# Kernel optimization log

Measured on AMD Instinct MI355X. Metric: run time of the kernel, lower is better.

## Reference

```python
import jax, jax.numpy as jnp
import numpy as np

N_EXPERTS, D_MODEL, D_FF = 8, 1024, 2048
N_TOKENS, TOP_K = 4 * 2048, 2


def setup_inputs() -> dict:
    key = jax.random.key(0)
    ks = jax.random.split(key, 6)
    std = (1.0 / 3.0) ** 0.5
    return {
        "x": jax.random.normal(ks[0], (4, 2048, D_MODEL), dtype=jnp.float32),
        "expert_indices": jax.random.randint(ks[1], (N_TOKENS, TOP_K), 0, N_EXPERTS, dtype=jnp.int64),
        "expert_weights": jax.random.uniform(ks[2], (N_TOKENS, TOP_K), dtype=jnp.float32),
        "w1": jax.random.normal(ks[3], (N_EXPERTS, D_MODEL, D_FF), dtype=jnp.float32) * (std / D_MODEL ** 0.5),
        "w2": jax.random.normal(ks[4], (N_EXPERTS, D_MODEL, D_FF), dtype=jnp.float32) * (std / D_MODEL ** 0.5),
        "w3": jax.random.normal(ks[5], (N_EXPERTS, D_FF, D_MODEL), dtype=jnp.float32) * (std / D_FF ** 0.5),
    }


def reference(x, expert_indices, expert_weights, w1, w2, w3):
    input_shape = x.shape
    d = x.shape[-1]
    xt = x.reshape(-1, d)                      # [N, d_model]
    n_tokens = xt.shape[0]
    n_experts = w1.shape[0]
    # Dense routing matrix [N, E]: sum of top-k weights per (token, expert).
    # Equivalent to the original's per-pair scatter (index_add) combine.
    route = jnp.zeros((n_tokens, n_experts), dtype=xt.dtype)
    route = route.at[jnp.arange(n_tokens)[:, None], expert_indices].add(expert_weights)

    def step(acc, ws):
        w1e, w2e, w3e, re = ws
        hidden = jax.nn.silu(xt @ w1e) * (xt @ w2e)   # SwiGLU [N, d_ff]
        return acc + re[:, None] * (hidden @ w3e), None

    out, _ = jax.lax.scan(step, jnp.zeros_like(xt), (w1, w2, w3, route.T))
    return out.reshape(input_shape)
```

## Files before the change

### kernel.cpp

```cpp
#include <hip/hip_runtime.h>
#include <cstdint>

typedef unsigned short u16;
typedef u16 u16x8 __attribute__((ext_vector_type(8)));
typedef __bf16 bf16x8 __attribute__((ext_vector_type(8)));
typedef float f32x4 __attribute__((ext_vector_type(4)));

#define DEV static __device__ __forceinline__

constexpr int NT = 8192;
constexpr int NP = NT * 2;
constexpr int NE = 8;
constexpr int DM = 1024;
constexpr int DF = 2048;
constexpr int MAXS = 17664;
constexpr int MAXT256 = 71;
constexpr int MAXT128 = 136;
constexpr int NWG1 = 8 * 142;
constexpr int NWG2 = 8 * MAXT128;
constexpr int NTRANS = 24 * 512;
constexpr int NPREP = MAXS + NTRANS;

DEV u16 f2bf(float f) {
  uint32_t u = __builtin_bit_cast(uint32_t, f);
  u += 0x7fffu + ((u >> 16) & 1u);
  return (u16)(u >> 16);
}

DEV void gload16(const void* g, void* l) {
  __builtin_amdgcn_global_load_lds((const __attribute__((address_space(1))) void*)g,
                                   (__attribute__((address_space(3))) void*)l, 16, 0, 0);
}

DEV bf16x8 ldfrag(const char* p) { return __builtin_bit_cast(bf16x8, *(const u16x8*)p); }

DEV f32x4 MFMA(bf16x8 a, bf16x8 b, f32x4 c) {
  return __builtin_amdgcn_mfma_f32_16x16x32_bf16(a, b, c, 0, 0, 0);
}

__global__ void k_route(const int* __restrict__ eidx, const float* __restrict__ ew,
                        int* meta, int* slot_token, float* slot_weight, int* pair_slot) {
  __shared__ int cnt[NE], cur[NE], off[NE];
  const int tid = threadIdx.x;
  if (tid < NE) { cnt[tid] = 0; cur[tid] = 0; }
  __syncthreads();
  for (int p = tid; p < NP; p += 1024) atomicAdd(&cnt[eidx[p] & 7], 1);
  __syncthreads();
  if (tid == 0) {
    int o = 0, t2 = 0, t1 = 0;
    for (int e = 0; e < NE; ++e) {
      off[e] = o; meta[e] = cnt[e]; meta[16 + e] = o;
      const int c = cnt[e];
      o += ((c + 127) >> 7) << 7;
      for (int mt = 0; mt * 256 < c; ++mt) meta[32 + t2++] = e | (mt << 8);
      for (int mt = 0; mt * 128 < c; ++mt) meta[128 + t1++] = e | (mt << 8);
    }
    meta[24] = o; meta[25] = t2; meta[26] = t1;
  }
  __syncthreads();
  for (int s = tid; s < MAXS; s += 1024) slot_token[s] = -1;
  __syncthreads();
  for (int p = tid; p < NP; p += 1024) {
    const int e = eidx[p] & 7;
    const int pos = off[e] + atomicAdd(&cur[e], 1);
    slot_token[pos]  = p >> 1;
    slot_weight[pos] = ew[p];
    pair_slot[p] = pos;
  }
}

__global__ void k_prep(const float* __restrict__ x, const int* __restrict__ slot_token,
                       u16* __restrict__ Xg,
                       const float* __restrict__ w1, const float* __restrict__ w2,
                       const float* __restrict__ w3, u16* __restrict__ w1T,
                       u16* __restrict__ w2T, u16* __restrict__ w3T) {
  __shared__ u16 tile[64][72];
  const int bid = blockIdx.x;
  const int t = threadIdx.x;

  if (bid < MAXS) {
    const int tok = slot_token[bid];
    const int c = t * 4;
    alignas(8) u16 b[4] = {0, 0, 0, 0};
    if (tok >= 0) {
      const float4 v = *reinterpret_cast<const float4*>(x + (size_t)tok * DM + c);
      b[0] = f2bf(v.x); b[1] = f2bf(v.y); b[2] = f2bf(v.z); b[3] = f2bf(v.w);
    }
    *reinterpret_cast<uint2*>(Xg + (size_t)bid * DM + c) = *reinterpret_cast<const uint2*>(b);
    return;
  }

  const int fid = bid - MAXS;
  const int z = fid >> 9;
  const int id = fid & 511;
  const int which = z >> 3, e = z & 7;
  const float* s; u16* d; int K, N, n0, k0;
  const size_t mo = (size_t)e * DM * DF;
  if (which == 0)      { s = w1 + mo; d = w1T + mo; K = DM; N = DF; n0 = (id & 31) * 64; k0 = (id >> 5) * 64; }
  else if (which == 1) { s = w2 + mo; d = w2T + mo; K = DM; N = DF; n0 = (id & 31) * 64; k0 = (id >> 5) * 64; }
  else                 { s = w3 + mo; d = w3T + mo; K = DF; N = DM; n0 = (id & 15) * 64; k0 = (id >> 4) * 64; }

  const int r = t >> 4, cb = (t & 15) * 4;
#pragma unroll
  for (int it = 0; it < 4; ++it) {
    const float4 v = *reinterpret_cast<const float4*>(s + (size_t)(k0 + r + it * 16) * N + n0 + cb);
    tile[r + it * 16][cb + 0] = f2bf(v.x);
    tile[r + it * 16][cb + 1] = f2bf(v.y);
    tile[r + it * 16][cb + 2] = f2bf(v.z);
    tile[r + it * 16][cb + 3] = f2bf(v.w);
  }
  __syncthreads();
  const int nl = t >> 2, ks = (t & 3) * 16;
  alignas(16) u16 vals[16];
#pragma unroll
  for (int j = 0; j < 16; ++j) vals[j] = tile[ks + j][nl];
  u16* dp = d + (size_t)(n0 + nl) * K + k0 + ks;
  *reinterpret_cast<uint4*>(dp)     = *reinterpret_cast<const uint4*>(vals);
  *reinterpret_cast<uint4*>(dp + 8) = *reinterpret_cast<const uint4*>(vals + 8);
}

__global__ __launch_bounds__(512, 2)
void k_gemm1(const u16* __restrict__ Xg, const u16* __restrict__ w1T, const u16* __restrict__ w2T,
             u16* __restrict__ H, const int* __restrict__ meta) {
  const int bid = blockIdx.x;
  const int xcd = bid & 7;
  const int local = bid >> 3;
  const int ti = local >> 1;
  if (ti >= meta[25]) return;
  const int n0 = (xcd * 2 + (local & 1)) * 128;
  const int ent = meta[32 + ti];
  const int e = ent & 255, mt = ent >> 8;
  const int base = meta[16 + e];
  const int cntp = meta[17 + e] - base;

  __shared__ __align__(16) char sm[2][65536];

  const int tid = threadIdx.x;
  const int lane = tid & 63;
  const int w = tid >> 6;
  const int wr = w >> 2, wc = w & 3;
  const int lrow = lane & 15, lk = lane >> 4;
  const int SX = lrow & 7;
  int cofs[2];
  cofs[0] = ((0 * 4 + lk) ^ SX) * 16;
  cofs[1] = ((1 * 4 + lk) ^ SX) * 16;
  const int Abase  = (wr * 128 + lrow) * 128;
  const int B1base = 32768 + (wc * 32 + lrow) * 128;
  const int B2base = B1base + 16384;

  const int srow8 = tid >> 3;
  const int scolw = ((tid & 7) ^ (srow8 & 7)) * 16;

  const char* AgT = (const char*)(Xg + (size_t)(base + mt * 256) * DM) + (size_t)srow8 * 2048 + scolw;
  const char* B1T = (const char*)(w1T + ((size_t)e * DF + n0) * DM)    + (size_t)srow8 * 2048 + scolw;
  const char* B2T = (const char*)(w2T + ((size_t)e * DF + n0) * DM)    + (size_t)srow8 * 2048 + scolw;

  f32x4 acc1[8][2] = {};
  f32x4 acc2[8][2] = {};

  auto SP = [&](char* d, size_t kb, int q) {
    switch (q) {
      case 0: gload16(AgT + kb,          d + tid * 16);
              gload16(AgT + 131072 + kb, d + 8192  + tid * 16); break;
      case 1: gload16(AgT + 262144 + kb, d + 16384 + tid * 16);
              gload16(AgT + 393216 + kb, d + 24576 + tid * 16); break;
      case 2: gload16(B1T + kb,          d + 32768 + tid * 16);
              gload16(B1T + 131072 + kb, d + 40960 + tid * 16); break;
      case 3: gload16(B2T + kb,          d + 49152 + tid * 16);
              gload16(B2T + 131072 + kb, d + 57344 + tid * 16); break;
    }
  };

  bf16x8 b1f[2][2], b2f[2][2];

  auto LDA4 = [&](const char* s, int mh, int ks, bf16x8* a) {
#pragma unroll
    for (int j = 0; j < 4; ++j)
      a[j] = ldfrag(s + Abase + mh * 8192 + j * 2048 + cofs[ks]);
  };
  auto MF16 = [&](int mh, int ks, const bf16x8* a) {
    __builtin_amdgcn_s_setprio(1);
#pragma unroll
    for (int j = 0; j < 4; ++j)
#pragma unroll
      for (int n = 0; n < 2; ++n) {
        acc1[mh * 4 + j][n] = MFMA(a[j], b1f[n][ks], acc1[mh * 4 + j][n]);
        acc2[mh * 4 + j][n] = MFMA(a[j], b2f[n][ks], acc2[mh * 4 + j][n]);
      }
    __builtin_amdgcn_s_setprio(0);
  };

  SP(sm[0], 0, 0); SP(sm[0], 0, 1); SP(sm[0], 0, 2); SP(sm[0], 0, 3);

  for (int kt = 0; kt < 16; ++kt) {
    const char* s = sm[kt & 1];
    char* d = sm[(kt + 1) & 1];
    const size_t kbn = (size_t)((kt + 1 < 16) ? kt + 1 : 15) * 128;
    bf16x8 a[4];

    SP(d, kbn, 0);
    asm volatile("s_waitcnt vmcnt(2)" ::: "memory");
    __builtin_amdgcn_s_barrier();
#pragma unroll
    for (int n = 0; n < 2; ++n)
#pragma unroll
      for (int s2 = 0; s2 < 2; ++s2) {
        b1f[n][s2] = ldfrag(s + B1base + n * 2048 + cofs[s2]);
        b2f[n][s2] = ldfrag(s + B2base + n * 2048 + cofs[s2]);
      }
    LDA4(s, 0, 0, a);
    MF16(0, 0, a);
    __builtin_amdgcn_s_barrier();

    LDA4(s, 1, 0, a);
    SP(d, kbn, 1);
    __builtin_amdgcn_s_barrier();
    MF16(1, 0, a);
    __builtin_amdgcn_s_barrier();

    LDA4(s, 0, 1, a);
    SP(d, kbn, 2);
    __builtin_amdgcn_s_barrier();
    MF16(0, 1, a);
    __builtin_amdgcn_s_barrier();

    LDA4(s, 1, 1, a);
    SP(d, kbn, 3);
    __builtin_amdgcn_s_barrier();
    MF16(1, 1, a);
    __builtin_amdgcn_s_barrier();
  }

  u16* Hrow = H + (size_t)(base + mt * 256) * DF + n0;
#pragma unroll
  for (int m = 0; m < 8; ++m)
#pragma unroll
    for (int r = 0; r < 4; ++r) {
      const int rloc = wr * 128 + m * 16 + lk * 4 + r;
      if (mt * 256 + rloc >= cntp) continue;
      u16* hp = Hrow + (size_t)rloc * DF + wc * 32 + lrow;
#pragma unroll
      for (int n = 0; n < 2; ++n) {
        const float h1 = acc1[m][n][r], h2 = acc2[m][n][r];
        const float sv = h1 / (1.f + __expf(-h1)) * h2;
        hp[n * 16] = f2bf(sv);
      }
    }
}

__global__ __launch_bounds__(256, 2)
void k_gemm2(const u16* __restrict__ H, const u16* __restrict__ w3T, const int* __restrict__ meta,
             const float* __restrict__ slot_weight, u16* __restrict__ O) {
  const int bid = blockIdx.x;
  const int ti = bid >> 3;
  if (ti >= meta[26]) return;
  const int n0 = (bid & 7) * 128;
  const int ent = meta[128 + ti];
  const int e = ent & 255, mt = ent >> 8;
  const int base = meta[16 + e];

  __shared__ __align__(16) char sm[2][32768];

  const int tid = threadIdx.x;
  const int lane = tid & 63;
  const int w = tid >> 6;
  const int wr = w >> 1, wc = w & 1;
  const int lrow = lane & 15, lk = lane >> 4;
  const int SX = lrow & 7;
  int cofs[2];
  cofs[0] = ((0 * 4 + lk) ^ SX) * 16;
  cofs[1] = ((1 * 4 + lk) ^ SX) * 16;
  const int Abase = (wr * 64 + lrow) * 128;
  const int Bbase = 16384 + (wc * 64 + lrow) * 128;

  const int srow = tid >> 3;
  const int scolw = ((tid & 7) ^ (srow & 7)) * 16;

  const char* AgT = (const char*)(H + (size_t)(base + mt * 128) * DF) + (size_t)srow * 4096 + scolw;
  const char* BgT = (const char*)(w3T + ((size_t)e * DM + n0) * DF)   + (size_t)srow * 4096 + scolw;

  f32x4 acc[4][4] = {};

  auto SPA = [&](char* d, size_t kb) {
#pragma unroll
    for (int c = 0; c < 4; ++c)
      gload16(AgT + (size_t)c * 131072 + kb, d + c * 4096 + tid * 16);
  };
  auto SPB = [&](char* d, size_t kb) {
#pragma unroll
    for (int c = 0; c < 4; ++c)
      gload16(BgT + (size_t)c * 131072 + kb, d + 16384 + c * 4096 + tid * 16);
  };

  bf16x8 bf[4][2];

  auto LDA4 = [&](const char* s, int ks, bf16x8* a) {
#pragma unroll
    for (int j = 0; j < 4; ++j)
      a[j] = ldfrag(s + Abase + j * 2048 + cofs[ks]);
  };
  auto MF16 = [&](int ks, const bf16x8* a) {
    __builtin_amdgcn_s_setprio(1);
#pragma unroll
    for (int j = 0; j < 4; ++j)
#pragma unroll
      for (int n = 0; n < 4; ++n)
        acc[j][n] = MFMA(a[j], bf[n][ks], acc[j][n]);
    __builtin_amdgcn_s_setprio(0);
  };

  SPA(sm[0], 0); SPB(sm[0], 0);

  for (int kt = 0; kt < 32; ++kt) {
    const char* s = sm[kt & 1];
    char* d = sm[(kt + 1) & 1];
    const size_t kbn = (size_t)((kt + 1 < 32) ? kt + 1 : 31) * 128;
    bf16x8 a[4];

    SPA(d, kbn);
    asm volatile("s_waitcnt vmcnt(4)" ::: "memory");
    __builtin_amdgcn_s_barrier();
#pragma unroll
    for (int n = 0; n < 4; ++n)
#pragma unroll
      for (int s2 = 0; s2 < 2; ++s2)
        bf[n][s2] = ldfrag(s + Bbase + n * 2048 + cofs[s2]);
    LDA4(s, 0, a);
    MF16(0, a);
    __builtin_amdgcn_s_barrier();

    LDA4(s, 1, a);
    SPB(d, kbn);
    __builtin_amdgcn_s_barrier();
    MF16(1, a);
    __builtin_amdgcn_s_barrier();
  }

  const int sb = base + mt * 128;
#pragma unroll
  for (int m = 0; m < 4; ++m)
#pragma unroll
    for (int r = 0; r < 4; ++r) {
      const int rloc = wr * 64 + m * 16 + lk * 4 + r;
      const float wgt = slot_weight[sb + rloc];
      u16* op = O + (size_t)(sb + rloc) * DM + n0 + wc * 64 + lrow;
#pragma unroll
      for (int n = 0; n < 4; ++n)
        op[n * 16] = f2bf(wgt * acc[m][n][r]);
    }
}

__global__ void k_combine(const u16* __restrict__ O, const int* __restrict__ pair_slot,
                          float* __restrict__ out) {
  const int t = blockIdx.x;
  const int c = threadIdx.x * 4;
  const int sa = pair_slot[2 * t], sb = pair_slot[2 * t + 1];
  const uint2 va = *reinterpret_cast<const uint2*>(O + (size_t)sa * DM + c);
  const uint2 vb = *reinterpret_cast<const uint2*>(O + (size_t)sb * DM + c);
  float4 r;
  r.x = __builtin_bit_cast(float, va.x << 16)          + __builtin_bit_cast(float, vb.x << 16);
  r.y = __builtin_bit_cast(float, va.x & 0xffff0000u)  + __builtin_bit_cast(float, vb.x & 0xffff0000u);
  r.z = __builtin_bit_cast(float, va.y << 16)          + __builtin_bit_cast(float, vb.y << 16);
  r.w = __builtin_bit_cast(float, va.y & 0xffff0000u)  + __builtin_bit_cast(float, vb.y & 0xffff0000u);
  *reinterpret_cast<float4*>(out + (size_t)t * DM + c) = r;
}

extern "C" void kernel_launch(void* const* d_in, const int* in_sizes, int n_in,
                              void* d_out, int out_size, void* d_ws, size_t ws_size,
                              hipStream_t stream) {
  const float* x  = (const float*)d_in[0];
  const int* eidx = (const int*)d_in[1];
  const float* ew = (const float*)d_in[2];
  const float* w1 = (const float*)d_in[3];
  const float* w2 = (const float*)d_in[4];
  const float* w3 = (const float*)d_in[5];
  float* out = (float*)d_out;
  char* ws = (char*)d_ws;

  int* meta          = (int*)ws;
  int* pair_slot     = (int*)(ws + 2048);
  int* slot_token    = (int*)(ws + 2048 + 65536);
  float* slot_weight = (float*)(ws + 2048 + 65536 + (size_t)MAXS * 4);
  size_t off = 2048 + 65536 + (size_t)MAXS * 8;
  u16* Xg  = (u16*)(ws + off); off += (size_t)MAXS * DM * 2;
  u16* w1T = (u16*)(ws + off); off += (size_t)NE * DM * DF * 2;
  u16* w2T = (u16*)(ws + off); off += (size_t)NE * DM * DF * 2;
  u16* w3T = (u16*)(ws + off); off += (size_t)NE * DM * DF * 2;
  u16* H   = (u16*)(ws + off);
  u16* O   = Xg;

  k_route<<<1, 1024, 0, stream>>>(eidx, ew, meta, slot_token, slot_weight, pair_slot);
  k_prep<<<NPREP, 256, 0, stream>>>(x, slot_token, Xg, w1, w2, w3, w1T, w2T, w3T);
  k_gemm1<<<NWG1, 512, 0, stream>>>(Xg, w1T, w2T, H, meta);
  k_gemm2<<<NWG2, 256, 0, stream>>>(H, w3T, meta, slot_weight, O);
  k_combine<<<NT, 256, 0, stream>>>(O, pair_slot, out);
}
```

Baseline: 373.0 us.

## Fuse routing into prep kernel and gather token rows inside gemm1 via row offsets

Folds the single-block routing kernel into block 0 of the prep kernel, which removes one launch. Instead of materializing a permuted bf16 copy of x per slot, prep now converts x once per token, plus one zero row used for padding. gemm1 then gathers rows through a per-slot byte-offset table during its global-to-LDS loads. This cuts the prep write traffic from 17664 rows to 8193 rows, but the A-operand loads become indirect gathers. Because routing now runs concurrently with the other prep blocks, it relies on gemm1 being launched after prep completes.

```diff
diff --git a/kernel.cpp b/kernel.cpp
--- a/kernel.cpp
+++ b/kernel.cpp
@@ -14,12 +14,11 @@
 constexpr int DM = 1024;
 constexpr int DF = 2048;
 constexpr int MAXS = 17664;
-constexpr int MAXT256 = 71;
 constexpr int MAXT128 = 136;
 constexpr int NWG1 = 8 * 142;
 constexpr int NWG2 = 8 * MAXT128;
 constexpr int NTRANS = 24 * 512;
-constexpr int NPREP = MAXS + NTRANS;
+constexpr int NPREP = 1 + NT + NTRANS;
 
 DEV u16 f2bf(float f) {
   uint32_t u = __builtin_bit_cast(uint32_t, f);
@@ -38,59 +37,58 @@
   return __builtin_amdgcn_mfma_f32_16x16x32_bf16(a, b, c, 0, 0, 0);
 }
 
-__global__ void k_route(const int* __restrict__ eidx, const float* __restrict__ ew,
-                        int* meta, int* slot_token, float* slot_weight, int* pair_slot) {
-  __shared__ int cnt[NE], cur[NE], off[NE];
-  const int tid = threadIdx.x;
-  if (tid < NE) { cnt[tid] = 0; cur[tid] = 0; }
-  __syncthreads();
-  for (int p = tid; p < NP; p += 1024) atomicAdd(&cnt[eidx[p] & 7], 1);
-  __syncthreads();
-  if (tid == 0) {
-    int o = 0, t2 = 0, t1 = 0;
-    for (int e = 0; e < NE; ++e) {
-      off[e] = o; meta[e] = cnt[e]; meta[16 + e] = o;
-      const int c = cnt[e];
-      o += ((c + 127) >> 7) << 7;
-      for (int mt = 0; mt * 256 < c; ++mt) meta[32 + t2++] = e | (mt << 8);
-      for (int mt = 0; mt * 128 < c; ++mt) meta[128 + t1++] = e | (mt << 8);
-    }
-    meta[24] = o; meta[25] = t2; meta[26] = t1;
-  }
-  __syncthreads();
-  for (int s = tid; s < MAXS; s += 1024) slot_token[s] = -1;
-  __syncthreads();
-  for (int p = tid; p < NP; p += 1024) {
-    const int e = eidx[p] & 7;
-    const int pos = off[e] + atomicAdd(&cur[e], 1);
-    slot_token[pos]  = p >> 1;
-    slot_weight[pos] = ew[p];
-    pair_slot[p] = pos;
-  }
-}
-
-__global__ void k_prep(const float* __restrict__ x, const int* __restrict__ slot_token,
-                       u16* __restrict__ Xg,
+__global__ void k_prep(const int* __restrict__ eidx, const float* __restrict__ ew,
+                       int* meta, int* rowoff, float* slot_weight, int* pair_slot,
+                       const float* __restrict__ x, u16* __restrict__ Xb,
                        const float* __restrict__ w1, const float* __restrict__ w2,
                        const float* __restrict__ w3, u16* __restrict__ w1T,
                        u16* __restrict__ w2T, u16* __restrict__ w3T) {
-  __shared__ u16 tile[64][72];
   const int bid = blockIdx.x;
   const int t = threadIdx.x;
 
-  if (bid < MAXS) {
-    const int tok = slot_token[bid];
-    const int c = t * 4;
-    alignas(8) u16 b[4] = {0, 0, 0, 0};
-    if (tok >= 0) {
-      const float4 v = *reinterpret_cast<const float4*>(x + (size_t)tok * DM + c);
-      b[0] = f2bf(v.x); b[1] = f2bf(v.y); b[2] = f2bf(v.z); b[3] = f2bf(v.w);
+  if (bid == 0) {
+    __shared__ int cnt[NE], cur[NE], off8[NE];
+    if (t < NE) { cnt[t] = 0; cur[t] = 0; }
+    __syncthreads();
+    for (int p = t; p < NP; p += 256) atomicAdd(&cnt[eidx[p] & 7], 1);
+    __syncthreads();
+    if (t == 0) {
+      int o = 0, t2 = 0, t1 = 0;
+      for (int e = 0; e < NE; ++e) {
+        off8[e] = o; meta[16 + e] = o;
+        const int c = cnt[e];
+        o += ((c + 127) >> 7) << 7;
+        for (int mt = 0; mt * 256 < c; ++mt) meta[32 + t2++] = e | (mt << 8);
+        for (int mt = 0; mt * 128 < c; ++mt) meta[128 + t1++] = e | (mt << 8);
+      }
+      meta[24] = o; meta[25] = t2; meta[26] = t1;
     }
-    *reinterpret_cast<uint2*>(Xg + (size_t)bid * DM + c) = *reinterpret_cast<const uint2*>(b);
+    __syncthreads();
+    for (int s = t; s < MAXS; s += 256) rowoff[s] = NT * (DM * 2);
+    __syncthreads();
+    for (int p = t; p < NP; p += 256) {
+      const int e = eidx[p] & 7;
+      const int pos = off8[e] + atomicAdd(&cur[e], 1);
+      rowoff[pos] = (p >> 1) * (DM * 2);
+      slot_weight[pos] = ew[p];
+      pair_slot[p] = pos;
+    }
+    uint32_t* zr = (uint32_t*)(Xb + (size_t)NT * DM);
+    for (int i = t; i < 512; i += 256) zr[i] = 0;
     return;
   }
 
-  const int fid = bid - MAXS;
+  if (bid <= NT) {
+    const int row = bid - 1;
+    const int c = t * 4;
+    const float4 v = *reinterpret_cast<const float4*>(x + (size_t)row * DM + c);
+    alignas(8) u16 b[4] = {f2bf(v.x), f2bf(v.y), f2bf(v.z), f2bf(v.w)};
+    *reinterpret_cast<uint2*>(Xb + (size_t)row * DM + c) = *reinterpret_cast<const uint2*>(b);
+    return;
+  }
+
+  __shared__ u16 tile[64][72];
+  const int fid = bid - 1 - NT;
   const int z = fid >> 9;
   const int id = fid & 511;
   const int which = z >> 3, e = z & 7;
@@ -120,7 +118,8 @@
 }
 
 __global__ __launch_bounds__(512, 2)
-void k_gemm1(const u16* __restrict__ Xg, const u16* __restrict__ w1T, const u16* __restrict__ w2T,
+void k_gemm1(const u16* __restrict__ Xb, const int* __restrict__ rowoff,
+             const u16* __restrict__ w1T, const u16* __restrict__ w2T,
              u16* __restrict__ H, const int* __restrict__ meta) {
   const int bid = blockIdx.x;
   const int xcd = bid & 7;
@@ -151,19 +150,25 @@
   const int srow8 = tid >> 3;
   const int scolw = ((tid & 7) ^ (srow8 & 7)) * 16;
 
-  const char* AgT = (const char*)(Xg + (size_t)(base + mt * 256) * DM) + (size_t)srow8 * 2048 + scolw;
-  const char* B1T = (const char*)(w1T + ((size_t)e * DF + n0) * DM)    + (size_t)srow8 * 2048 + scolw;
-  const char* B2T = (const char*)(w2T + ((size_t)e * DF + n0) * DM)    + (size_t)srow8 * 2048 + scolw;
+  const int sb = base + mt * 256;
+  const int* ro = rowoff + sb + srow8;
+  const char* Xc = (const char*)Xb + scolw;
+  const char* A0 = Xc + ro[0];
+  const char* A1 = Xc + ro[64];
+  const char* A2 = Xc + ro[128];
+  const char* A3 = Xc + ro[192];
+  const char* B1T = (const char*)(w1T + ((size_t)e * DF + n0) * DM) + (size_t)srow8 * 2048 + scolw;
+  const char* B2T = (const char*)(w2T + ((size_t)e * DF + n0) * DM) + (size_t)srow8 * 2048 + scolw;
 
   f32x4 acc1[8][2] = {};
   f32x4 acc2[8][2] = {};
 
   auto SP = [&](char* d, size_t kb, int q) {
     switch (q) {
-      case 0: gload16(AgT + kb,          d + tid * 16);
-              gload16(AgT + 131072 + kb, d + 8192  + tid * 16); break;
-      case 1: gload16(AgT + 262144 + kb, d + 16384 + tid * 16);
-              gload16(AgT + 393216 + kb, d + 24576 + tid * 16); break;
+      case 0: gload16(A0 + kb, d + tid * 16);
+              gload16(A1 + kb, d + 8192  + tid * 16); break;
+      case 1: gload16(A2 + kb, d + 16384 + tid * 16);
+              gload16(A3 + kb, d + 24576 + tid * 16); break;
       case 2: gload16(B1T + kb,          d + 32768 + tid * 16);
               gload16(B1T + 131072 + kb, d + 40960 + tid * 16); break;
       case 3: gload16(B2T + kb,          d + 49152 + tid * 16);
@@ -379,19 +384,19 @@
 
   int* meta          = (int*)ws;
   int* pair_slot     = (int*)(ws + 2048);
-  int* slot_token    = (int*)(ws + 2048 + 65536);
+  int* rowoff        = (int*)(ws + 2048 + 65536);
   float* slot_weight = (float*)(ws + 2048 + 65536 + (size_t)MAXS * 4);
   size_t off = 2048 + 65536 + (size_t)MAXS * 8;
-  u16* Xg  = (u16*)(ws + off); off += (size_t)MAXS * DM * 2;
+  u16* Xb  = (u16*)(ws + off); off += (size_t)(NT + 1) * DM * 2;
+  u16* O   = (u16*)(ws + off); off += (size_t)MAXS * DM * 2;
   u16* w1T = (u16*)(ws + off); off += (size_t)NE * DM * DF * 2;
   u16* w2T = (u16*)(ws + off); off += (size_t)NE * DM * DF * 2;
   u16* w3T = (u16*)(ws + off); off += (size_t)NE * DM * DF * 2;
   u16* H   = (u16*)(ws + off);
-  u16* O   = Xg;
-
-  k_route<<<1, 1024, 0, stream>>>(eidx, ew, meta, slot_token, slot_weight, pair_slot);
-  k_prep<<<NPREP, 256, 0, stream>>>(x, slot_token, Xg, w1, w2, w3, w1T, w2T, w3T);
-  k_gemm1<<<NWG1, 512, 0, stream>>>(Xg, w1T, w2T, H, meta);
+
+  k_prep<<<NPREP, 256, 0, stream>>>(eidx, ew, meta, rowoff, slot_weight, pair_slot,
+                                    x, Xb, w1, w2, w3, w1T, w2T, w3T);
+  k_gemm1<<<NWG1, 512, 0, stream>>>(Xb, rowoff, w1T, w2T, H, meta);
   k_gemm2<<<NWG2, 256, 0, stream>>>(H, w3T, meta, slot_weight, O);
   k_combine<<<NT, 256, 0, stream>>>(O, pair_slot, out);
 }
```

Measured after the change: 386.3 us. 3.5% more time.
